# Kernel optimization log

Hardware: AMD Instinct MI355X
Metric: run time of the kernel (lower is better)

Reference implementation:

```python
import jax, jax.numpy as jnp
import numpy as np

N_NODES = 100000    # nodes in river network
N_PATHS = 1000000   # number of (src, dst) routing paths
MAX_DELAY = 16
DT = 1.0
CASCADE = 1.0
T = int(MAX_DELAY / DT)        # expanded time window (assert in original)
E = 8000000                    # total flattened path-node entries


def setup_inputs() -> dict:
    key = jax.random.key(0)
    k1, k2, k3 = jax.random.split(key, 3)
    params = jax.random.uniform(k1, (N_NODES,), dtype=jnp.float32)
    path_idxs = jnp.sort(jax.random.randint(k2, (E,), 0, N_PATHS, dtype=jnp.int32))
    path_nodes = jax.random.randint(k3, (E,), 0, N_NODES, dtype=jnp.int32)
    return {"params": params, "path_idxs": path_idxs, "path_nodes": path_nodes}


def reference(params, path_idxs, path_nodes):
    # irf_fn 'linear_storage': per-node linear-reservoir impulse response h(t)=exp(-t/k)/k
    k = params + 0.5                                  # storage const in [0.5, 1.5)
    t = jnp.arange(T, dtype=params.dtype) * DT        # [T]
    irfs = jnp.exp(-t[None, :] / k[:, None]) / k[:, None]   # [N, T]
    # frequency domain
    irfs_freq = jnp.fft.rfft(irfs, n=T, axis=-1)      # [N, F] complex
    # irf_agg 'log_triton': cascade-combine IRFs along each path = product of
    # transfer functions, done in log domain: gather logs, segment-sum per path.
    log_freq = jnp.log(irfs_freq)                     # [N, F] complex log
    gathered = log_freq[path_nodes]                   # [E, F] irregular gather
    agg_re = jax.ops.segment_sum(gathered.real, path_idxs, num_segments=N_PATHS)
    agg_im = jax.ops.segment_sum(gathered.imag, path_idxs, num_segments=N_PATHS)
    agg_log = (agg_re + 1j * agg_im) * CASCADE        # [P, F]
    irfs_freq_agg = jnp.exp(agg_log)
    # back to time domain
    irfs_agg = jnp.fft.irfft(irfs_freq_agg, n=T, axis=-1)   # [P, T]
    irfs_agg = jax.nn.relu(irfs_agg)
    irfs_agg = jnp.flip(irfs_agg, -1)                 # sampler.phi_k is identity for dt=1
    irfs_agg = irfs_agg / jnp.sum(irfs_agg, -1, keepdims=True)
    return irfs_agg                                   # COO values; coords scatter is a storage step
```

## Files before the change

### kernel.cpp

```cpp
#include <hip/hip_runtime.h>
#include <math.h>

#define N_NODES  100000
#define N_PATHS  1000000
#define E_TOT    8000000
#define NW_TOT   (E_TOT / 4)
#define TAB_U32  25000
#define EB       1024
#define EPT      8
#define PB       256
#define KW       9

#define RMIN 0.135330f
#define RMAX 0.513420f
#define QSCALE (255.0f / (RMAX - RMIN))
#define DEQ    ((RMAX - RMIN) / 255.0f)

typedef int   v4i __attribute__((ext_vector_type(4)));
typedef float v4f __attribute__((ext_vector_type(4)));
typedef unsigned long long u64;

__device__ __constant__ float COS16[16] = {
  1.0f,  0.92387953f,  0.70710678f,  0.38268343f,  0.0f, -0.38268343f, -0.70710678f, -0.92387953f,
 -1.0f, -0.92387953f, -0.70710678f, -0.38268343f,  0.0f,  0.38268343f,  0.70710678f,  0.92387953f };
__device__ __constant__ float SIN16[16] = {
  0.0f,  0.38268343f,  0.70710678f,  0.92387953f,  1.0f,  0.92387953f,  0.70710678f,  0.38268343f,
  0.0f, -0.38268343f, -0.70710678f, -0.92387953f, -1.0f, -0.92387953f, -0.70710678f, -0.38268343f };

__global__ void node_rq_kernel(const float* __restrict__ params,
                               unsigned char* __restrict__ rtab_q) {
    int n = blockIdx.x * blockDim.x + threadIdx.x;
    if (n >= N_NODES) return;
    float k = params[n] + 0.5f;
    float r = expf(-1.0f / k);
    float q = (r - RMIN) * QSCALE;
    q = fminf(fmaxf(q + 0.5f, 0.0f), 255.0f);
    rtab_q[n] = (unsigned char)q;
}

__device__ __forceinline__ void put_bounds(int a, int b, int e, int* __restrict__ start) {
    for (int p = a + 1; p <= b; ++p) start[p] = e;
}

__global__ __launch_bounds__(EB) void epass_kernel(const int* __restrict__ pidx,
                                                   const int* __restrict__ pnode,
                                                   const unsigned int* __restrict__ rtab_q,
                                                   int* __restrict__ start,
                                                   unsigned char* __restrict__ r8_all) {
    __shared__ unsigned int tab[TAB_U32];
    const unsigned char* tabb = (const unsigned char*)tab;
    int tid = threadIdx.x;
    for (int i = tid; i < TAB_U32; i += EB) tab[i] = rtab_q[i];
    __syncthreads();

    int base_q = blockIdx.x * EB * EPT;
#pragma unroll
    for (int g = 0; g < EPT; g++) {
        int q = base_q + g * EB + tid;
        if (q >= NW_TOT) break;
        int e = q * 4;
        v4i v = *((const v4i*)pidx + q);
        v4i w = *((const v4i*)pnode + q);
        uchar4 r;
        r.x = tabb[w.x];
        r.y = tabb[w.y];
        r.z = tabb[w.z];
        r.w = tabb[w.w];
        ((uchar4*)r8_all)[q] = r;
        int prev = __shfl_up((int)v.w, 1);
        if ((tid & 63) == 0) prev = (e == 0) ? -1 : pidx[e - 1];
        put_bounds(prev, v.x, e,     start);
        put_bounds(v.x,  v.y, e + 1, start);
        put_bounds(v.y,  v.z, e + 2, start);
        put_bounds(v.z,  v.w, e + 3, start);
        if (e + 4 == E_TOT) {
            for (int p = v.w + 1; p <= N_PATHS; ++p) start[p] = E_TOT;
        }
    }
}

__device__ __forceinline__ void quad_step(unsigned grp, int rem,
                                          float& d0, float& d8,
                                          float dr[7], float di[7]) {
    float ra = fmaf((float)(grp & 255u), DEQ, RMIN);
    float rb = (rem > 1) ? fmaf((float)((grp >> 8) & 255u), DEQ, RMIN) : 0.0f;
    float rc = (rem > 2) ? fmaf((float)((grp >> 16) & 255u), DEQ, RMIN) : 0.0f;
    float rd = (rem > 3) ? fmaf((float)(grp >> 24), DEQ, RMIN) : 0.0f;
    float sab = ra + rb, qab = ra * rb;
    float scd = rc + rd, qcd = rc * rd;
    float e1 = sab + scd;
    float e2 = fmaf(sab, scd, qab + qcd);
    float e3 = fmaf(qab, scd, qcd * sab);
    float e4 = qab * qcd;
#pragma unroll
    for (int f = 1; f <= 7; f++) {
        float tr = fmaf(-e1, COS16[f], 1.0f);
        tr = fmaf( e2, COS16[(2 * f) & 15], tr);
        tr = fmaf(-e3, COS16[(3 * f) & 15], tr);
        tr = fmaf( e4, COS16[(4 * f) & 15], tr);
        float ti = e1 * SIN16[f];
        ti = fmaf(-e2, SIN16[(2 * f) & 15], ti);
        ti = fmaf( e3, SIN16[(3 * f) & 15], ti);
        ti = fmaf(-e4, SIN16[(4 * f) & 15], ti);
        float a = dr[f - 1], b = di[f - 1];
        dr[f - 1] = fmaf(a, tr, -b * ti);
        di[f - 1] = fmaf(a, ti,  b * tr);
    }
    d0 *= ((1.0f - e1) + (e2 - e3)) + e4;
    d8 *= ((1.0f + e1) + (e2 + e3)) + e4;
}

__global__ __launch_bounds__(PB) void path_kernel(const int* __restrict__ start,
                                                  const unsigned int* __restrict__ r8w,
                                                  float* __restrict__ out) {
    __shared__ v4f lds_o[PB * 4];
    int tid = threadIdx.x;
    int p = blockIdx.x * PB + tid;
    int L = tid & 63;
    v4f* lw = lds_o + (tid >> 6) * 256;

    if (p < N_PATHS) {
        int s0 = start[p];
        int s1 = start[p + 1];
        int len = s1 - s0;
        int nq = (len + 3) >> 2;
        int a0 = s0 >> 2;
        unsigned sh = (unsigned)(s0 & 3) * 8u;

        unsigned wv[KW];
#pragma unroll
        for (int i = 0; i < KW; ++i) {
            int idx = a0 + i;
            wv[i] = r8w[idx < NW_TOT ? idx : (NW_TOT - 1)];
        }

        float d0 = 1.0f, d8 = 1.0f;
        float dr[7], di[7];
#pragma unroll
        for (int f = 0; f < 7; f++) { dr[f] = 1.0f; di[f] = 0.0f; }

#pragma unroll
        for (int q = 0; q < KW - 1; ++q) {
            if (q < nq) {
                unsigned grp = (unsigned)((((u64)wv[q + 1] << 32) |
                                           (u64)wv[q]) >> sh);
                quad_step(grp, len - 4 * q, d0, d8, dr, di);
            }
        }
        if (len > 32) {
            unsigned cur = wv[KW - 1];
            for (int q = KW - 1; q < nq; ++q) {
                int w = a0 + q + 1;
                unsigned nxt = (w < NW_TOT) ? r8w[w] : 0u;
                unsigned grp = (unsigned)((((u64)nxt << 32) | (u64)cur) >> sh);
                cur = nxt;
                quad_step(grp, len - 4 * q, d0, d8, dr, di);
            }
        }

        float Xr[8], Xi[8];
        Xr[0] = 1.0f; Xi[0] = 0.0f;
#pragma unroll
        for (int f = 1; f < 8; f++) {
            float a = dr[f - 1], b = di[f - 1];
            float m = fmaf(a, a, b * b);
            float inv = d0 * __builtin_amdgcn_rcpf(m);
            Xr[f] =  a * inv;
            Xi[f] = -b * inv;
        }
        float X8 = d0 * __builtin_amdgcn_rcpf(d8);

        float xt[16];
        float c0 = 0.0f, c8s = 0.0f;
#pragma unroll
        for (int f = 1; f < 8; f++) {
            c0 += 2.0f * Xr[f];
            c8s += (f & 1) ? -2.0f * Xr[f] : 2.0f * Xr[f];
        }
        xt[0] = fmaxf((Xr[0] + X8 + c0) * (1.0f / 16.0f), 0.0f);
        xt[8] = fmaxf((Xr[0] + X8 + c8s) * (1.0f / 16.0f), 0.0f);
        float ssum = xt[0] + xt[8];
#pragma unroll
        for (int t = 1; t < 8; t++) {
            float Ct = 0.0f, St = 0.0f;
#pragma unroll
            for (int f = 1; f < 8; f++) {
                int kk = (f * t) & 15;
                Ct = fmaf(2.0f * Xr[f], COS16[kk], Ct);
                St = fmaf(2.0f * Xi[f], SIN16[kk], St);
            }
            float base = Xr[0] + ((t & 1) ? -X8 : X8) + Ct;
            float xa = fmaxf((base - St) * (1.0f / 16.0f), 0.0f);
            float xb = fmaxf((base + St) * (1.0f / 16.0f), 0.0f);
            xt[t] = xa;
            xt[16 - t] = xb;
            ssum += xa + xb;
        }

        float invs = __builtin_amdgcn_rcpf(ssum);
        lw[L * 4 + (0 ^ (L & 3))] =
            (v4f){ xt[15] * invs, xt[14] * invs, xt[13] * invs, xt[12] * invs };
        lw[L * 4 + (1 ^ (L & 3))] =
            (v4f){ xt[11] * invs, xt[10] * invs, xt[9]  * invs, xt[8]  * invs };
        lw[L * 4 + (2 ^ (L & 3))] =
            (v4f){ xt[7]  * invs, xt[6]  * invs, xt[5]  * invs, xt[4]  * invs };
        lw[L * 4 + (3 ^ (L & 3))] =
            (v4f){ xt[3]  * invs, xt[2]  * invs, xt[1]  * invs, xt[0]  * invs };
    }

    __syncthreads();

    int P0 = (blockIdx.x * PB) + (tid & ~63);
    if (P0 < N_PATHS) {
        v4f* outw = (v4f*)out + (size_t)P0 * 4;
#pragma unroll
        for (int k = 0; k < 4; ++k) {
            int m = k * 64 + L;
            int q = m >> 2;
            int c = m & 3;
            outw[m] = lw[q * 4 + (c ^ (q & 3))];
        }
    }
}

extern "C" void kernel_launch(void* const* d_in, const int* in_sizes, int n_in,
                              void* d_out, int out_size, void* d_ws, size_t ws_size,
                              hipStream_t stream) {
    const float* params = (const float*)d_in[0];
    const int* path_idxs = (const int*)d_in[1];
    const int* path_nodes = (const int*)d_in[2];
    float* out = (float*)d_out;

    size_t off_rq    = 0;
    size_t off_start = (off_rq + (size_t)N_NODES + 1023) & ~(size_t)1023;
    size_t off_r8    = (off_start + (size_t)(N_PATHS + 1) * 4 + 1023) & ~(size_t)1023;

    unsigned char* rtab_q = (unsigned char*)d_ws + off_rq;
    int* start = (int*)((char*)d_ws + off_start);
    unsigned char* r8_all = (unsigned char*)d_ws + off_r8;

    {
        int threads = 256;
        int blocks = (N_NODES + threads - 1) / threads;
        node_rq_kernel<<<blocks, threads, 0, stream>>>(params, rtab_q);
    }
    {
        int per_block = EB * EPT;
        int blocks = (NW_TOT + per_block - 1) / per_block;
        epass_kernel<<<blocks, EB, 0, stream>>>(path_idxs, path_nodes,
                                                (const unsigned int*)rtab_q,
                                                start, r8_all);
    }
    {
        int blocks = (N_PATHS + PB - 1) / PB;
        path_kernel<<<blocks, PB, 0, stream>>>(start, (const unsigned int*)r8_all, out);
    }
}
```

Before: 139.4 us.

## Split edge pass into separate boundary and gather kernels with prefetch

Splits the fused edge pass into two kernels. The first computes path start offsets from path_idxs using small 256-thread blocks with no shared table. The second gathers quantized node ratios and issues the path_nodes loads before and during the shared-table fill, so global latency overlaps the table copy. This stops the boundary work from paying for the 100KB LDS table, at the cost of one extra kernel launch.

```diff
diff --git a/kernel.cpp b/kernel.cpp
--- a/kernel.cpp
+++ b/kernel.cpp
@@ -6,8 +6,10 @@
 #define E_TOT    8000000
 #define NW_TOT   (E_TOT / 4)
 #define TAB_U32  25000
-#define EB       1024
-#define EPT      8
+#define BB       256
+#define BPT      8
+#define GB       1024
+#define GPT      8
 #define PB       256
 #define KW       9
 
@@ -42,31 +44,16 @@
     for (int p = a + 1; p <= b; ++p) start[p] = e;
 }
 
-__global__ __launch_bounds__(EB) void epass_kernel(const int* __restrict__ pidx,
-                                                   const int* __restrict__ pnode,
-                                                   const unsigned int* __restrict__ rtab_q,
-                                                   int* __restrict__ start,
-                                                   unsigned char* __restrict__ r8_all) {
-    __shared__ unsigned int tab[TAB_U32];
-    const unsigned char* tabb = (const unsigned char*)tab;
+__global__ __launch_bounds__(BB) void bound_kernel(const int* __restrict__ pidx,
+                                                   int* __restrict__ start) {
     int tid = threadIdx.x;
-    for (int i = tid; i < TAB_U32; i += EB) tab[i] = rtab_q[i];
-    __syncthreads();
-
-    int base_q = blockIdx.x * EB * EPT;
-#pragma unroll
-    for (int g = 0; g < EPT; g++) {
-        int q = base_q + g * EB + tid;
+    int base_q = blockIdx.x * (BB * BPT);
+#pragma unroll
+    for (int g = 0; g < BPT; g++) {
+        int q = base_q + g * BB + tid;
         if (q >= NW_TOT) break;
         int e = q * 4;
         v4i v = *((const v4i*)pidx + q);
-        v4i w = *((const v4i*)pnode + q);
-        uchar4 r;
-        r.x = tabb[w.x];
-        r.y = tabb[w.y];
-        r.z = tabb[w.z];
-        r.w = tabb[w.w];
-        ((uchar4*)r8_all)[q] = r;
         int prev = __shfl_up((int)v.w, 1);
         if ((tid & 63) == 0) prev = (e == 0) ? -1 : pidx[e - 1];
         put_bounds(prev, v.x, e,     start);
@@ -75,6 +62,57 @@
         put_bounds(v.z,  v.w, e + 3, start);
         if (e + 4 == E_TOT) {
             for (int p = v.w + 1; p <= N_PATHS; ++p) start[p] = E_TOT;
+        }
+    }
+}
+
+__global__ __launch_bounds__(GB) void gather_kernel(const int* __restrict__ pnode,
+                                                    const unsigned int* __restrict__ rtab_q,
+                                                    unsigned char* __restrict__ r8_all) {
+    __shared__ v4i tab4[TAB_U32 / 4];
+    const unsigned char* tabb = (const unsigned char*)tab4;
+    int tid = threadIdx.x;
+    int base_q = blockIdx.x * (GB * GPT);
+
+    if (base_q + GB * GPT <= NW_TOT) {
+        const v4i* pnode4 = (const v4i*)pnode;
+        v4i wa[4];
+#pragma unroll
+        for (int g = 0; g < 4; ++g) wa[g] = pnode4[base_q + g * GB + tid];
+        for (int i = tid; i < TAB_U32 / 4; i += GB)
+            tab4[i] = ((const v4i*)rtab_q)[i];
+        __syncthreads();
+
+        v4i wb[4];
+#pragma unroll
+        for (int g = 0; g < 4; ++g) wb[g] = pnode4[base_q + (g + 4) * GB + tid];
+
+#pragma unroll
+        for (int g = 0; g < 8; ++g) {
+            v4i w = (g < 4) ? wa[g & 3] : wb[g & 3];
+            int q = base_q + g * GB + tid;
+            uchar4 r;
+            r.x = tabb[w.x];
+            r.y = tabb[w.y];
+            r.z = tabb[w.z];
+            r.w = tabb[w.w];
+            ((uchar4*)r8_all)[q] = r;
+        }
+    } else {
+        for (int i = tid; i < TAB_U32 / 4; i += GB)
+            tab4[i] = ((const v4i*)rtab_q)[i];
+        __syncthreads();
+#pragma unroll
+        for (int g = 0; g < GPT; g++) {
+            int q = base_q + g * GB + tid;
+            if (q >= NW_TOT) break;
+            v4i w = *((const v4i*)pnode + q);
+            uchar4 r;
+            r.x = tabb[w.x];
+            r.y = tabb[w.y];
+            r.z = tabb[w.z];
+            r.w = tabb[w.w];
+            ((uchar4*)r8_all)[q] = r;
         }
     }
 }
@@ -245,11 +283,16 @@
         node_rq_kernel<<<blocks, threads, 0, stream>>>(params, rtab_q);
     }
     {
-        int per_block = EB * EPT;
+        int per_block = BB * BPT;
         int blocks = (NW_TOT + per_block - 1) / per_block;
-        epass_kernel<<<blocks, EB, 0, stream>>>(path_idxs, path_nodes,
-                                                (const unsigned int*)rtab_q,
-                                                start, r8_all);
+        bound_kernel<<<blocks, BB, 0, stream>>>(path_idxs, start);
+    }
+    {
+        int per_block = GB * GPT;
+        int blocks = (NW_TOT + per_block - 1) / per_block;
+        gather_kernel<<<blocks, GB, 0, stream>>>(path_nodes,
+                                                 (const unsigned int*)rtab_q,
+                                                 r8_all);
     }
     {
         int blocks = (N_PATHS + PB - 1) / PB;
```

Result: slower. 143.0 us (+2.5%).
